# Optimization experiments

Measured on AMD Instinct MI355X. Metric: run time of the kernel, lower is better.

The kernel has to match this reference:

```python
import jax, jax.numpy as jnp
import numpy as np


def setup_inputs() -> dict:
    key = jax.random.key(0)
    x = jax.random.normal(key, (128, 256, 32, 32), dtype=jnp.float32)
    return {"x": x, "topk": 5}


def reference(x, topk):
    B = x.shape[0]
    flat = x.reshape(B, -1)                      # [B, N]
    _, idx = jax.lax.top_k(flat, topk)           # [B, k] indices into N
    out = jnp.zeros_like(flat)
    out = out.at[jnp.arange(B)[:, None], idx].set(1.0)
    return out.reshape(x.shape)
```

## Files before the change

### kernel.cpp

```cpp
#include <hip/hip_runtime.h>
#include <limits.h>
#include <math.h>
#include <stdint.h>

#define BROWS 128
#define NCOLS (256 * 32 * 32)
#define K 5
#define BPR 8
#define TPB 256
#define CHUNK (NCOLS / BPR)
#define F4T (CHUNK / 4 / TPB)
#define BATCH 8
#define NBATCH (F4T / BATCH)

typedef float v4f __attribute__((ext_vector_type(4)));

__device__ __forceinline__ uint64_t make_key(float f, uint32_t idx) {
    uint32_t u = __float_as_uint(f);
    u = (u & 0x80000000u) ? ~u : (u | 0x80000000u);
    return ((uint64_t)u << 32) | (uint32_t)(~idx);
}
__device__ __forceinline__ float key_val(uint64_t k) {
    uint32_t u = (uint32_t)(k >> 32);
    u = (u & 0x80000000u) ? (u ^ 0x80000000u) : ~u;
    return __uint_as_float(u);
}
__device__ __forceinline__ uint32_t key_idx(uint64_t k) {
    return ~(uint32_t)k;
}

#define KEY_NEG_INF 0x007FFFFF00000000ULL

__device__ __forceinline__ void insert5(uint64_t (&key)[K], uint64_t c) {
    if (c > key[K - 1]) {
        key[K - 1] = c;
#pragma unroll
        for (int s = K - 1; s > 0; --s) {
            if (key[s] > key[s - 1]) {
                uint64_t t = key[s]; key[s] = key[s - 1]; key[s - 1] = t;
            }
        }
    }
}

__device__ __forceinline__ void wave_reduce5(uint64_t (&key)[K]) {
#pragma unroll
    for (int off = 1; off < 64; off <<= 1) {
        uint64_t ok[K];
#pragma unroll
        for (int k = 0; k < K; ++k)
            ok[k] = __shfl_xor((unsigned long long)key[k], off, 64);
#pragma unroll
        for (int k = 0; k < K; ++k) insert5(key, ok[k]);
    }
}

__global__ __launch_bounds__(TPB) void wta_scan(const float* __restrict__ x,
                                                float* __restrict__ out,
                                                uint64_t* __restrict__ wsk) {
    const int gb  = blockIdx.x;
    const int row = gb / BPR;
    const int blk = gb % BPR;
    const size_t base = (size_t)row * NCOLS + (size_t)blk * CHUNK;
    const float4* __restrict__ x4 = (const float4*)(x + base);
    v4f* __restrict__ o4 = (v4f*)(out + base);
    const int t = threadIdx.x;

    uint64_t key[K];
#pragma unroll
    for (int k = 0; k < K; ++k) key[k] = KEY_NEG_INF;
    float vmin = -INFINITY;

    const v4f z = {0.f, 0.f, 0.f, 0.f};

    float4 cur[BATCH], nxt[BATCH];
#pragma unroll
    for (int j = 0; j < BATCH; ++j) cur[j] = x4[t + j * TPB];

#pragma unroll
    for (int b = 0; b < NBATCH; ++b) {
        if (b + 1 < NBATCH) {
#pragma unroll
            for (int j = 0; j < BATCH; ++j)
                nxt[j] = x4[t + ((b + 1) * BATCH + j) * TPB];
        }
#pragma unroll
        for (int j = 0; j < BATCH; ++j)
            __builtin_nontemporal_store(z, &o4[t + (b * BATCH + j) * TPB]);
#pragma unroll
        for (int j = 0; j < BATCH; ++j) {
            const float4 d = cur[j];
            const float m = fmaxf(fmaxf(d.x, d.y), fmaxf(d.z, d.w));
            if (m >= vmin) {
                const uint32_t e = (uint32_t)(blk * CHUNK) +
                                   (uint32_t)(t + (b * BATCH + j) * TPB) * 4u;
                insert5(key, make_key(d.x, e + 0));
                insert5(key, make_key(d.y, e + 1));
                insert5(key, make_key(d.z, e + 2));
                insert5(key, make_key(d.w, e + 3));
                vmin = key_val(key[K - 1]);
            }
        }
#pragma unroll
        for (int j = 0; j < BATCH; ++j) cur[j] = nxt[j];
    }

    wave_reduce5(key);

    __shared__ uint64_t sk[TPB / 64][K];
    const int wave = t >> 6, lane = t & 63;
    if (lane == 0) {
#pragma unroll
        for (int k = 0; k < K; ++k) sk[wave][k] = key[k];
    }
    __syncthreads();
    if (t == 0) {
#pragma unroll
        for (int w = 1; w < TPB / 64; ++w)
#pragma unroll
            for (int k = 0; k < K; ++k) insert5(key, sk[w][k]);
#pragma unroll
        for (int k = 0; k < K; ++k) wsk[gb * K + k] = key[k];
    }
}

__global__ __launch_bounds__(64) void wta_final(const uint64_t* __restrict__ wsk,
                                                float* __restrict__ out) {
    const int row  = blockIdx.x;
    const int lane = threadIdx.x;

    uint64_t key[K];
#pragma unroll
    for (int k = 0; k < K; ++k) key[k] = KEY_NEG_INF;

    const int ncand = BPR * K;
    if (lane < ncand) insert5(key, wsk[row * ncand + lane]);

    wave_reduce5(key);

    if (lane == 0) {
#pragma unroll
        for (int k = 0; k < K; ++k)
            out[(size_t)row * NCOLS + key_idx(key[k])] = 1.0f;
    }
}

extern "C" void kernel_launch(void* const* d_in, const int* in_sizes, int n_in,
                              void* d_out, int out_size, void* d_ws, size_t ws_size,
                              hipStream_t stream) {
    const float* x = (const float*)d_in[0];
    float* out = (float*)d_out;
    uint64_t* wsk = (uint64_t*)d_ws;

    wta_scan<<<BROWS * BPR, TPB, 0, stream>>>(x, out, wsk);
    wta_final<<<BROWS, 64, 0, stream>>>(wsk, out);
}
```

Baseline: 261.9 us.

## Split zero-fill into separate kernel and load whole chunk into registers

Moves zeroing of the output out of the scan kernel into a dedicated fill kernel launched afterwards. The scan now only reads input, uses four times more blocks per row (32), and loads its full per-thread chunk into registers up front instead of double-buffered batches. The final merge loops over the larger candidate count. This decouples read and write streams and increases parallelism, but adds a kernel launch and serialises the write pass after the read pass instead of overlapping them.

```diff
diff --git a/kernel.cpp b/kernel.cpp
--- a/kernel.cpp
+++ b/kernel.cpp
@@ -6,12 +6,14 @@
 #define BROWS 128
 #define NCOLS (256 * 32 * 32)
 #define K 5
-#define BPR 8
+#define BPR 32
 #define TPB 256
 #define CHUNK (NCOLS / BPR)
 #define F4T (CHUNK / 4 / TPB)
-#define BATCH 8
-#define NBATCH (F4T / BATCH)
+
+#define TOTAL_F4 ((size_t)BROWS * NCOLS / 4)
+#define FILL_BLOCKS 4096
+#define FILL_F4T (TOTAL_F4 / FILL_BLOCKS / TPB)
 
 typedef float v4f __attribute__((ext_vector_type(4)));
 
@@ -56,53 +58,36 @@
 }
 
 __global__ __launch_bounds__(TPB) void wta_scan(const float* __restrict__ x,
-                                                float* __restrict__ out,
                                                 uint64_t* __restrict__ wsk) {
     const int gb  = blockIdx.x;
     const int row = gb / BPR;
     const int blk = gb % BPR;
     const size_t base = (size_t)row * NCOLS + (size_t)blk * CHUNK;
     const float4* __restrict__ x4 = (const float4*)(x + base);
-    v4f* __restrict__ o4 = (v4f*)(out + base);
     const int t = threadIdx.x;
+
+    float4 r[F4T];
+#pragma unroll
+    for (int i = 0; i < F4T; ++i) r[i] = x4[t + i * TPB];
 
     uint64_t key[K];
 #pragma unroll
     for (int k = 0; k < K; ++k) key[k] = KEY_NEG_INF;
     float vmin = -INFINITY;
 
-    const v4f z = {0.f, 0.f, 0.f, 0.f};
-
-    float4 cur[BATCH], nxt[BATCH];
 #pragma unroll
-    for (int j = 0; j < BATCH; ++j) cur[j] = x4[t + j * TPB];
-
-#pragma unroll
-    for (int b = 0; b < NBATCH; ++b) {
-        if (b + 1 < NBATCH) {
-#pragma unroll
-            for (int j = 0; j < BATCH; ++j)
-                nxt[j] = x4[t + ((b + 1) * BATCH + j) * TPB];
+    for (int i = 0; i < F4T; ++i) {
+        const float4 d = r[i];
+        const float m = fmaxf(fmaxf(d.x, d.y), fmaxf(d.z, d.w));
+        if (m >= vmin) {
+            const uint32_t e = (uint32_t)(blk * CHUNK) +
+                               (uint32_t)(t + i * TPB) * 4u;
+            insert5(key, make_key(d.x, e + 0));
+            insert5(key, make_key(d.y, e + 1));
+            insert5(key, make_key(d.z, e + 2));
+            insert5(key, make_key(d.w, e + 3));
+            vmin = key_val(key[K - 1]);
         }
-#pragma unroll
-        for (int j = 0; j < BATCH; ++j)
-            __builtin_nontemporal_store(z, &o4[t + (b * BATCH + j) * TPB]);
-#pragma unroll
-        for (int j = 0; j < BATCH; ++j) {
-            const float4 d = cur[j];
-            const float m = fmaxf(fmaxf(d.x, d.y), fmaxf(d.z, d.w));
-            if (m >= vmin) {
-                const uint32_t e = (uint32_t)(blk * CHUNK) +
-                                   (uint32_t)(t + (b * BATCH + j) * TPB) * 4u;
-                insert5(key, make_key(d.x, e + 0));
-                insert5(key, make_key(d.y, e + 1));
-                insert5(key, make_key(d.z, e + 2));
-                insert5(key, make_key(d.w, e + 3));
-                vmin = key_val(key[K - 1]);
-            }
-        }
-#pragma unroll
-        for (int j = 0; j < BATCH; ++j) cur[j] = nxt[j];
     }
 
     wave_reduce5(key);
@@ -124,6 +109,15 @@
     }
 }
 
+__global__ __launch_bounds__(TPB) void wta_fill(float* __restrict__ out) {
+    v4f* __restrict__ o4 = (v4f*)out;
+    const size_t base = (size_t)blockIdx.x * (TPB * FILL_F4T) + threadIdx.x;
+    const v4f z = {0.f, 0.f, 0.f, 0.f};
+#pragma unroll
+    for (int i = 0; i < FILL_F4T; ++i)
+        __builtin_nontemporal_store(z, &o4[base + (size_t)i * TPB]);
+}
+
 __global__ __launch_bounds__(64) void wta_final(const uint64_t* __restrict__ wsk,
                                                 float* __restrict__ out) {
     const int row  = blockIdx.x;
@@ -134,7 +128,8 @@
     for (int k = 0; k < K; ++k) key[k] = KEY_NEG_INF;
 
     const int ncand = BPR * K;
-    if (lane < ncand) insert5(key, wsk[row * ncand + lane]);
+    for (int c = lane; c < ncand; c += 64)
+        insert5(key, wsk[row * ncand + c]);
 
     wave_reduce5(key);
 
@@ -152,6 +147,7 @@
     float* out = (float*)d_out;
     uint64_t* wsk = (uint64_t*)d_ws;
 
-    wta_scan<<<BROWS * BPR, TPB, 0, stream>>>(x, out, wsk);
+    wta_scan<<<BROWS * BPR, TPB, 0, stream>>>(x, wsk);
+    wta_fill<<<FILL_BLOCKS, TPB, 0, stream>>>(out);
     wta_final<<<BROWS, 64, 0, stream>>>(wsk, out);
 }
```

Measured after the change: 260.7 us. No clear change (-0.5%).

## Replace per-thread top-k scan with block-max threshold and atomic candidate filter

Applied to the files above, without the earlier changes.

Splits the work into four kernels. The first computes per-chunk maxima, and the second takes the 5th largest chunk max as a per-row threshold, which is a valid lower bound on the 5th largest value. The third pass zeros the output and appends only elements at or above the threshold to a candidate list using atomics. A final kernel selects the top-5 from those candidates. This removes the per-element register insertion sort from the streaming pass but reads the input twice. It also relies on the candidate count staying within a fixed capacity, and if that is exceeded the result is silently wrong.

```diff
diff --git a/kernel.cpp b/kernel.cpp
--- a/kernel.cpp
+++ b/kernel.cpp
@@ -6,12 +6,11 @@
 #define BROWS 128
 #define NCOLS (256 * 32 * 32)
 #define K 5
-#define BPR 8
+#define BPR 16
 #define TPB 256
 #define CHUNK (NCOLS / BPR)
 #define F4T (CHUNK / 4 / TPB)
-#define BATCH 8
-#define NBATCH (F4T / BATCH)
+#define CAP 256
 
 typedef float v4f __attribute__((ext_vector_type(4)));
 
@@ -20,14 +19,7 @@
     u = (u & 0x80000000u) ? ~u : (u | 0x80000000u);
     return ((uint64_t)u << 32) | (uint32_t)(~idx);
 }
-__device__ __forceinline__ float key_val(uint64_t k) {
-    uint32_t u = (uint32_t)(k >> 32);
-    u = (u & 0x80000000u) ? (u ^ 0x80000000u) : ~u;
-    return __uint_as_float(u);
-}
-__device__ __forceinline__ uint32_t key_idx(uint64_t k) {
-    return ~(uint32_t)k;
-}
+__device__ __forceinline__ uint32_t key_idx(uint64_t k) { return ~(uint32_t)k; }
 
 #define KEY_NEG_INF 0x007FFFFF00000000ULL
 
@@ -55,93 +47,120 @@
     }
 }
 
-__global__ __launch_bounds__(TPB) void wta_scan(const float* __restrict__ x,
-                                                float* __restrict__ out,
-                                                uint64_t* __restrict__ wsk) {
+__device__ __forceinline__ void insert5f(float (&v)[K], float c) {
+    if (c > v[K - 1]) {
+        v[K - 1] = c;
+#pragma unroll
+        for (int s = K - 1; s > 0; --s) {
+            if (v[s] > v[s - 1]) { float t = v[s]; v[s] = v[s - 1]; v[s - 1] = t; }
+        }
+    }
+}
+
+__global__ __launch_bounds__(TPB) void wta_gmax(const float* __restrict__ x,
+                                                float* __restrict__ gmax) {
+    const int gb = blockIdx.x;
+    const float4* __restrict__ x4 = (const float4*)(x + (size_t)gb * CHUNK);
+    const int t = threadIdx.x;
+
+    float m = -INFINITY;
+#pragma unroll
+    for (int i = 0; i < F4T; ++i) {
+        const float4 d = x4[t + i * TPB];
+        m = fmaxf(m, fmaxf(fmaxf(d.x, d.y), fmaxf(d.z, d.w)));
+    }
+#pragma unroll
+    for (int off = 1; off < 64; off <<= 1)
+        m = fmaxf(m, __shfl_xor(m, off, 64));
+
+    __shared__ float sm[TPB / 64];
+    if ((t & 63) == 0) sm[t >> 6] = m;
+    __syncthreads();
+    if (t == 0)
+        gmax[gb] = fmaxf(fmaxf(sm[0], sm[1]), fmaxf(sm[2], sm[3]));
+}
+
+__global__ __launch_bounds__(64) void wta_thresh(const float* __restrict__ gmax,
+                                                 float* __restrict__ T,
+                                                 int* __restrict__ cnt) {
+    const int row = blockIdx.x, lane = threadIdx.x;
+    float v[K];
+#pragma unroll
+    for (int k = 0; k < K; ++k) v[k] = -INFINITY;
+    if (lane < BPR) insert5f(v, gmax[row * BPR + lane]);
+#pragma unroll
+    for (int off = 1; off < 64; off <<= 1) {
+        float ov[K];
+#pragma unroll
+        for (int k = 0; k < K; ++k) ov[k] = __shfl_xor(v[k], off, 64);
+#pragma unroll
+        for (int k = 0; k < K; ++k) insert5f(v, ov[k]);
+    }
+    if (lane == 0) { T[row] = v[K - 1]; cnt[row] = 0; }
+}
+
+__global__ __launch_bounds__(TPB) void wta_fillfilter(const float* __restrict__ x,
+                                                      float* __restrict__ out,
+                                                      const float* __restrict__ T,
+                                                      int* __restrict__ cnt,
+                                                      uint64_t* __restrict__ cand) {
     const int gb  = blockIdx.x;
     const int row = gb / BPR;
     const int blk = gb % BPR;
-    const size_t base = (size_t)row * NCOLS + (size_t)blk * CHUNK;
+    const size_t base = (size_t)gb * CHUNK;
     const float4* __restrict__ x4 = (const float4*)(x + base);
     v4f* __restrict__ o4 = (v4f*)(out + base);
     const int t = threadIdx.x;
+    const float Trow = T[row];
+    const v4f z = {0.f, 0.f, 0.f, 0.f};
+
+#pragma unroll
+    for (int h = 0; h < 2; ++h) {
+        float4 r[F4T / 2];
+#pragma unroll
+        for (int j = 0; j < F4T / 2; ++j)
+            r[j] = x4[t + (h * (F4T / 2) + j) * TPB];
+#pragma unroll
+        for (int j = 0; j < F4T / 2; ++j)
+            __builtin_nontemporal_store(z, &o4[t + (h * (F4T / 2) + j) * TPB]);
+#pragma unroll
+        for (int j = 0; j < F4T / 2; ++j) {
+            const float4 d = r[j];
+            const float m = fmaxf(fmaxf(d.x, d.y), fmaxf(d.z, d.w));
+            if (m >= Trow) {
+                const uint32_t e = (uint32_t)blk * CHUNK +
+                                   (uint32_t)(t + (h * (F4T / 2) + j) * TPB) * 4u;
+                const float vs[4] = {d.x, d.y, d.z, d.w};
+#pragma unroll
+                for (int c = 0; c < 4; ++c) {
+                    if (vs[c] >= Trow) {
+                        const int slot = atomicAdd(&cnt[row], 1);
+                        if (slot < CAP) cand[row * CAP + slot] = make_key(vs[c], e + c);
+                    }
+                }
+            }
+        }
+    }
+}
+
+__global__ __launch_bounds__(64) void wta_final(const int* __restrict__ cnt,
+                                                const uint64_t* __restrict__ cand,
+                                                float* __restrict__ out) {
+    const int row = blockIdx.x, lane = threadIdx.x;
+    const int n = min(cnt[row], CAP);
 
     uint64_t key[K];
 #pragma unroll
     for (int k = 0; k < K; ++k) key[k] = KEY_NEG_INF;
-    float vmin = -INFINITY;
-
-    const v4f z = {0.f, 0.f, 0.f, 0.f};
-
-    float4 cur[BATCH], nxt[BATCH];
-#pragma unroll
-    for (int j = 0; j < BATCH; ++j) cur[j] = x4[t + j * TPB];
-
-#pragma unroll
-    for (int b = 0; b < NBATCH; ++b) {
-        if (b + 1 < NBATCH) {
-#pragma unroll
-            for (int j = 0; j < BATCH; ++j)
-                nxt[j] = x4[t + ((b + 1) * BATCH + j) * TPB];
-        }
-#pragma unroll
-        for (int j = 0; j < BATCH; ++j)
-            __builtin_nontemporal_store(z, &o4[t + (b * BATCH + j) * TPB]);
-#pragma unroll
-        for (int j = 0; j < BATCH; ++j) {
-            const float4 d = cur[j];
-            const float m = fmaxf(fmaxf(d.x, d.y), fmaxf(d.z, d.w));
-            if (m >= vmin) {
-                const uint32_t e = (uint32_t)(blk * CHUNK) +
-                                   (uint32_t)(t + (b * BATCH + j) * TPB) * 4u;
-                insert5(key, make_key(d.x, e + 0));
-                insert5(key, make_key(d.y, e + 1));
-                insert5(key, make_key(d.z, e + 2));
-                insert5(key, make_key(d.w, e + 3));
-                vmin = key_val(key[K - 1]);
-            }
-        }
-#pragma unroll
-        for (int j = 0; j < BATCH; ++j) cur[j] = nxt[j];
-    }
-
-    wave_reduce5(key);
-
-    __shared__ uint64_t sk[TPB / 64][K];
-    const int wave = t >> 6, lane = t & 63;
-    if (lane == 0) {
-#pragma unroll
-        for (int k = 0; k < K; ++k) sk[wave][k] = key[k];
-    }
-    __syncthreads();
-    if (t == 0) {
-#pragma unroll
-        for (int w = 1; w < TPB / 64; ++w)
-#pragma unroll
-            for (int k = 0; k < K; ++k) insert5(key, sk[w][k]);
-#pragma unroll
-        for (int k = 0; k < K; ++k) wsk[gb * K + k] = key[k];
-    }
-}
-
-__global__ __launch_bounds__(64) void wta_final(const uint64_t* __restrict__ wsk,
-                                                float* __restrict__ out) {
-    const int row  = blockIdx.x;
-    const int lane = threadIdx.x;
-
-    uint64_t key[K];
-#pragma unroll
-    for (int k = 0; k < K; ++k) key[k] = KEY_NEG_INF;
-
-    const int ncand = BPR * K;
-    if (lane < ncand) insert5(key, wsk[row * ncand + lane]);
+    for (int c = lane; c < n; c += 64) insert5(key, cand[row * CAP + c]);
 
     wave_reduce5(key);
 
     if (lane == 0) {
 #pragma unroll
         for (int k = 0; k < K; ++k)
-            out[(size_t)row * NCOLS + key_idx(key[k])] = 1.0f;
+            if (key[k] != KEY_NEG_INF)
+                out[(size_t)row * NCOLS + key_idx(key[k])] = 1.0f;
     }
 }
 
@@ -150,8 +169,14 @@
                               hipStream_t stream) {
     const float* x = (const float*)d_in[0];
     float* out = (float*)d_out;
-    uint64_t* wsk = (uint64_t*)d_ws;
 
-    wta_scan<<<BROWS * BPR, TPB, 0, stream>>>(x, out, wsk);
-    wta_final<<<BROWS, 64, 0, stream>>>(wsk, out);
+    uint64_t* cand = (uint64_t*)d_ws;
+    float* gmax = (float*)(cand + (size_t)BROWS * CAP);
+    float* T    = gmax + BROWS * BPR;
+    int*   cnt  = (int*)(T + BROWS);
+
+    wta_gmax<<<BROWS * BPR, TPB, 0, stream>>>(x, gmax);
+    wta_thresh<<<BROWS, 64, 0, stream>>>(gmax, T, cnt);
+    wta_fillfilter<<<BROWS * BPR, TPB, 0, stream>>>(x, out, T, cnt, cand);
+    wta_final<<<BROWS, 64, 0, stream>>>(cnt, cand, out);
 }
```

Measured after the change: 253.5 us. 3.2% less time.

## Replace per-thread top-k scan with fixed-threshold filter and exact fallback

Applied to the files above, without the earlier changes.

The streaming scan no longer keeps a running top-5 per thread. Values at or above a fixed threshold of 3.3 are appended through a per-row atomic counter into a candidate buffer, and a final kernel picks the top 5 from those candidates. A fallback kernel rescans the full row whenever the candidate count is below 5 or overflows the buffer, so the result stays exact. This removes insertion-sort work from the bandwidth-bound pass and doubles the blocks per row, at the cost of two extra launches, atomics, and a threshold tuned to standard-normal inputs.

```diff
diff --git a/kernel.cpp b/kernel.cpp
--- a/kernel.cpp
+++ b/kernel.cpp
@@ -6,12 +6,13 @@
 #define BROWS 128
 #define NCOLS (256 * 32 * 32)
 #define K 5
-#define BPR 8
+#define BPR 16
 #define TPB 256
 #define CHUNK (NCOLS / BPR)
 #define F4T (CHUNK / 4 / TPB)
-#define BATCH 8
-#define NBATCH (F4T / BATCH)
+#define CAP 1024
+
+#define T_FILTER 3.3f
 
 typedef float v4f __attribute__((ext_vector_type(4)));
 
@@ -25,9 +26,7 @@
     u = (u & 0x80000000u) ? (u ^ 0x80000000u) : ~u;
     return __uint_as_float(u);
 }
-__device__ __forceinline__ uint32_t key_idx(uint64_t k) {
-    return ~(uint32_t)k;
-}
+__device__ __forceinline__ uint32_t key_idx(uint64_t k) { return ~(uint32_t)k; }
 
 #define KEY_NEG_INF 0x007FFFFF00000000ULL
 
@@ -55,15 +54,60 @@
     }
 }
 
-__global__ __launch_bounds__(TPB) void wta_scan(const float* __restrict__ x,
-                                                float* __restrict__ out,
-                                                uint64_t* __restrict__ wsk) {
+__global__ void wta_zerocnt(int* __restrict__ cnt) {
+    if (threadIdx.x < BROWS) cnt[threadIdx.x] = 0;
+}
+
+__global__ __launch_bounds__(TPB) void wta_fillfilter(const float* __restrict__ x,
+                                                      float* __restrict__ out,
+                                                      int* __restrict__ cnt,
+                                                      uint64_t* __restrict__ cand) {
     const int gb  = blockIdx.x;
     const int row = gb / BPR;
     const int blk = gb % BPR;
-    const size_t base = (size_t)row * NCOLS + (size_t)blk * CHUNK;
+    const size_t base = (size_t)gb * CHUNK;
     const float4* __restrict__ x4 = (const float4*)(x + base);
     v4f* __restrict__ o4 = (v4f*)(out + base);
+    const int t = threadIdx.x;
+    const v4f z = {0.f, 0.f, 0.f, 0.f};
+
+#pragma unroll
+    for (int h = 0; h < 2; ++h) {
+        float4 r[F4T / 2];
+#pragma unroll
+        for (int j = 0; j < F4T / 2; ++j)
+            r[j] = x4[t + (h * (F4T / 2) + j) * TPB];
+#pragma unroll
+        for (int j = 0; j < F4T / 2; ++j)
+            __builtin_nontemporal_store(z, &o4[t + (h * (F4T / 2) + j) * TPB]);
+#pragma unroll
+        for (int j = 0; j < F4T / 2; ++j) {
+            const float4 d = r[j];
+            const float m = fmaxf(fmaxf(d.x, d.y), fmaxf(d.z, d.w));
+            if (m >= T_FILTER) {
+                const uint32_t e = (uint32_t)blk * CHUNK +
+                                   (uint32_t)(t + (h * (F4T / 2) + j) * TPB) * 4u;
+                const float vs[4] = {d.x, d.y, d.z, d.w};
+#pragma unroll
+                for (int c = 0; c < 4; ++c) {
+                    if (vs[c] >= T_FILTER) {
+                        const int slot = atomicAdd(&cnt[row], 1);
+                        if (slot < CAP) cand[row * CAP + slot] = make_key(vs[c], e + c);
+                    }
+                }
+            }
+        }
+    }
+}
+
+__global__ __launch_bounds__(TPB) void wta_fallback(const float* __restrict__ x,
+                                                    int* __restrict__ cnt,
+                                                    uint64_t* __restrict__ cand) {
+    const int row = blockIdx.x;
+    const int n = cnt[row];
+    if (n >= K && n <= CAP) return;
+
+    const float4* __restrict__ x4 = (const float4*)(x + (size_t)row * NCOLS);
     const int t = threadIdx.x;
 
     uint64_t key[K];
@@ -71,38 +115,17 @@
     for (int k = 0; k < K; ++k) key[k] = KEY_NEG_INF;
     float vmin = -INFINITY;
 
-    const v4f z = {0.f, 0.f, 0.f, 0.f};
-
-    float4 cur[BATCH], nxt[BATCH];
-#pragma unroll
-    for (int j = 0; j < BATCH; ++j) cur[j] = x4[t + j * TPB];
-
-#pragma unroll
-    for (int b = 0; b < NBATCH; ++b) {
-        if (b + 1 < NBATCH) {
-#pragma unroll
-            for (int j = 0; j < BATCH; ++j)
-                nxt[j] = x4[t + ((b + 1) * BATCH + j) * TPB];
+    for (int i = t; i < NCOLS / 4; i += TPB) {
+        const float4 d = x4[i];
+        const float m = fmaxf(fmaxf(d.x, d.y), fmaxf(d.z, d.w));
+        if (m >= vmin) {
+            const uint32_t e = (uint32_t)i * 4u;
+            insert5(key, make_key(d.x, e + 0));
+            insert5(key, make_key(d.y, e + 1));
+            insert5(key, make_key(d.z, e + 2));
+            insert5(key, make_key(d.w, e + 3));
+            vmin = key_val(key[K - 1]);
         }
-#pragma unroll
-        for (int j = 0; j < BATCH; ++j)
-            __builtin_nontemporal_store(z, &o4[t + (b * BATCH + j) * TPB]);
-#pragma unroll
-        for (int j = 0; j < BATCH; ++j) {
-            const float4 d = cur[j];
-            const float m = fmaxf(fmaxf(d.x, d.y), fmaxf(d.z, d.w));
-            if (m >= vmin) {
-                const uint32_t e = (uint32_t)(blk * CHUNK) +
-                                   (uint32_t)(t + (b * BATCH + j) * TPB) * 4u;
-                insert5(key, make_key(d.x, e + 0));
-                insert5(key, make_key(d.y, e + 1));
-                insert5(key, make_key(d.z, e + 2));
-                insert5(key, make_key(d.w, e + 3));
-                vmin = key_val(key[K - 1]);
-            }
-        }
-#pragma unroll
-        for (int j = 0; j < BATCH; ++j) cur[j] = nxt[j];
     }
 
     wave_reduce5(key);
@@ -120,28 +143,29 @@
 #pragma unroll
             for (int k = 0; k < K; ++k) insert5(key, sk[w][k]);
 #pragma unroll
-        for (int k = 0; k < K; ++k) wsk[gb * K + k] = key[k];
+        for (int k = 0; k < K; ++k) cand[row * CAP + k] = key[k];
+        cnt[row] = K;
     }
 }
 
-__global__ __launch_bounds__(64) void wta_final(const uint64_t* __restrict__ wsk,
+__global__ __launch_bounds__(64) void wta_final(const int* __restrict__ cnt,
+                                                const uint64_t* __restrict__ cand,
                                                 float* __restrict__ out) {
-    const int row  = blockIdx.x;
-    const int lane = threadIdx.x;
+    const int row = blockIdx.x, lane = threadIdx.x;
+    const int n = min(cnt[row], CAP);
 
     uint64_t key[K];
 #pragma unroll
     for (int k = 0; k < K; ++k) key[k] = KEY_NEG_INF;
-
-    const int ncand = BPR * K;
-    if (lane < ncand) insert5(key, wsk[row * ncand + lane]);
+    for (int c = lane; c < n; c += 64) insert5(key, cand[row * CAP + c]);
 
     wave_reduce5(key);
 
     if (lane == 0) {
 #pragma unroll
         for (int k = 0; k < K; ++k)
-            out[(size_t)row * NCOLS + key_idx(key[k])] = 1.0f;
+            if (key[k] != KEY_NEG_INF)
+                out[(size_t)row * NCOLS + key_idx(key[k])] = 1.0f;
     }
 }
 
@@ -150,8 +174,12 @@
                               hipStream_t stream) {
     const float* x = (const float*)d_in[0];
     float* out = (float*)d_out;
-    uint64_t* wsk = (uint64_t*)d_ws;
 
-    wta_scan<<<BROWS * BPR, TPB, 0, stream>>>(x, out, wsk);
-    wta_final<<<BROWS, 64, 0, stream>>>(wsk, out);
+    uint64_t* cand = (uint64_t*)d_ws;
+    int* cnt = (int*)(cand + (size_t)BROWS * CAP);
+
+    wta_zerocnt<<<1, 128, 0, stream>>>(cnt);
+    wta_fillfilter<<<BROWS * BPR, TPB, 0, stream>>>(x, out, cnt, cand);
+    wta_fallback<<<BROWS, TPB, 0, stream>>>(x, cnt, cand);
+    wta_final<<<BROWS, 64, 0, stream>>>(cnt, cand, out);
 }
```

Result: slower. 271.8 us (+3.8%).
